# Kernel tuning notes

Measured on AMD Instinct MI355X. Metric: run time of the kernel, lower is better.

The kernel has to match this reference:

```python
import jax, jax.numpy as jnp
import numpy as np

N_NODES = 50000
N_EDGES = 800000
D_IN = 64
D_HID = 64
N_GRAPHS = 64


def setup_inputs() -> dict:
    key = jax.random.key(0)
    ks = jax.random.split(key, 10)
    x = jax.random.normal(ks[0], (N_NODES, D_IN), dtype=jnp.float32)
    edge_index = jax.random.randint(ks[1], (2, N_EDGES), 0, N_NODES, dtype=jnp.int64)
    batch = jnp.sort(jax.random.randint(ks[2], (N_NODES,), 0, N_GRAPHS, dtype=jnp.int64))
    s1 = 1.0 / np.sqrt(D_IN)
    s2 = 1.0 / np.sqrt(D_HID)
    W1 = jax.random.uniform(ks[3], (D_IN, D_HID), jnp.float32, -s1, s1)
    b1 = jnp.zeros((D_HID,), jnp.float32)
    W2 = jax.random.uniform(ks[4], (D_HID, D_HID), jnp.float32, -s2, s2)
    b2 = jnp.zeros((D_HID,), jnp.float32)
    W3 = jax.random.uniform(ks[5], (D_HID, D_HID), jnp.float32, -s2, s2)
    b3 = jnpp = jnp.zeros((D_HID,), jnp.float32)
    return {"x": x, "edge_index": edge_index, "batch": batch,
            "W1": W1, "b1": b1, "W2": W2, "b2": b2, "W3": W3, "b3": b3}


def _gcn_norm(edge_index, num_nodes):
    # add self-loops, then symmetric normalization deg^-1/2 A_hat deg^-1/2
    loop = jnp.arange(num_nodes, dtype=edge_index.dtype)
    row = jnp.concatenate([edge_index[0], loop])  # source
    col = jnp.concatenate([edge_index[1], loop])  # target (aggregation index)
    deg = jax.ops.segment_sum(jnp.ones_like(col, dtype=jnp.float32), col,
                              num_segments=num_nodes)
    dinv = jnp.where(deg > 0, jax.lax.rsqrt(deg), 0.0)
    norm = dinv[row] * dinv[col]  # [E+N]
    return row, col, norm


def _gcn_conv(x, row, col, norm, W, b, num_nodes):
    h = x @ W                                   # [N, D] small GEMM
    msg = h[row] * norm[:, None]                # edge-wise gather + scale
    out = jax.ops.segment_sum(msg, col, num_segments=num_nodes)  # scatter-add
    return out + b


def reference(x, edge_index, batch, W1, b1, W2, b2, W3, b3):
    n = x.shape[0]
    row, col, norm = _gcn_norm(edge_index, n)
    h = jax.nn.relu(_gcn_conv(x, row, col, norm, W1, b1, n))
    h = jax.nn.relu(_gcn_conv(h, row, col, norm, W2, b2, n))
    h = jax.nn.relu(_gcn_conv(h, row, col, norm, W3, b3, n))
    # global_mean_pool over graphs
    sums = jax.ops.segment_sum(h, batch, num_segments=N_GRAPHS)
    cnt = jax.ops.segment_sum(jnp.ones((n,), jnp.float32), batch,
                              num_segments=N_GRAPHS)
    return sums / jnp.maximum(cnt, 1.0)[:, None]
```

## Files before the change

kernel.cpp:

```cpp
#include <hip/hip_runtime.h>

#define N_NODES   50000
#define N_EDGES   800000
#define DF        64
#define N_GRAPHS  64
#define NPAD      50176

#define ABLK 200
#define AEDG (N_EDGES/ABLK)
#define RSH  9
#define NREG 98
#define RPAD 128
#define CAP  12288

__global__ __launch_bounds__(256)
void k_hist(const int* __restrict__ col, int* __restrict__ H,
            float* __restrict__ pool) {
    __shared__ int h[RPAD];
    const int t = threadIdx.x, b = blockIdx.x;
    if (b == 0)
        for (int i = t; i < N_GRAPHS * DF; i += 256) pool[i] = 0.f;
    if (t < RPAD) h[t] = 0;
    __syncthreads();
    const int e0 = b * AEDG;
    for (int i = t; i < AEDG; i += 256)
        atomicAdd(&h[col[e0 + i] >> RSH], 1);
    __syncthreads();
    if (t < RPAD) H[t * ABLK + b] = h[t];
}

__global__ __launch_bounds__(256)
void k_scanH(const int* __restrict__ H, int* __restrict__ O,
             int* __restrict__ T) {
    __shared__ int s[256];
    const int t = threadIdx.x, r = blockIdx.x;
    int v = (t < ABLK) ? H[r * ABLK + t] : 0;
    s[t] = v; __syncthreads();
    #pragma unroll
    for (int off = 1; off < 256; off <<= 1) {
        int x = (t >= off) ? s[t - off] : 0;
        __syncthreads();
        s[t] += x;
        __syncthreads();
    }
    if (t < ABLK) O[r * ABLK + t] = s[t] - v;
    if (t == 255) T[r] = s[255];
}

__global__ __launch_bounds__(256)
void k_bin(const int* __restrict__ row, const int* __restrict__ col,
           const int* __restrict__ O, const int* __restrict__ T,
           unsigned* __restrict__ staging) {
    __shared__ int cur[RPAD];
    __shared__ int rs[RPAD];
    const int t = threadIdx.x, b = blockIdx.x;
    int v = 0;
    if (t < RPAD) { v = T[t]; rs[t] = v; }
    __syncthreads();
    #pragma unroll
    for (int off = 1; off < RPAD; off <<= 1) {
        int x = 0;
        if (t < RPAD && t >= off) x = rs[t - off];
        __syncthreads();
        if (t < RPAD) rs[t] += x;
        __syncthreads();
    }
    if (t < RPAD) cur[t] = O[t * ABLK + b] + (rs[t] - v);
    __syncthreads();
    const int e0 = b * AEDG;
    for (int i = t; i < AEDG; i += 256) {
        int c = col[e0 + i];
        int rr = row[e0 + i];
        int slot = atomicAdd(&cur[c >> RSH], 1);
        staging[slot] = ((unsigned)c << 16) | (unsigned)rr;
    }
}

__global__ __launch_bounds__(512)
void k_csr(const unsigned* __restrict__ staging, const int* __restrict__ T,
           int* __restrict__ offs, float* __restrict__ dinv,
           int* __restrict__ esrc) {
    __shared__ int hist[512];
    __shared__ int cur[512];
    __shared__ int img[CAP];
    __shared__ int rs[RPAD];
    __shared__ int sh_s0, sh_s1;
    const int t = threadIdx.x, r = blockIdx.x;
    int v = 0;
    if (t < RPAD) { v = T[t]; rs[t] = v; }
    __syncthreads();
    #pragma unroll
    for (int off = 1; off < RPAD; off <<= 1) {
        int x = 0;
        if (t < RPAD && t >= off) x = rs[t - off];
        __syncthreads();
        if (t < RPAD) rs[t] += x;
        __syncthreads();
    }
    if (t == r) { sh_s0 = rs[t] - v; sh_s1 = rs[t]; }
    hist[t] = 0;
    __syncthreads();
    const int s0 = sh_s0, s1 = sh_s1;
    for (int i = s0 + t; i < s1; i += 512) {
        int ln = (int)(staging[i] >> 16) - (r << RSH);
        atomicAdd(&hist[ln], 1);
    }
    __syncthreads();
    int myc = hist[t];
    #pragma unroll
    for (int off = 1; off < 512; off <<= 1) {
        int x = (t >= off) ? hist[t - off] : 0;
        __syncthreads();
        hist[t] += x;
        __syncthreads();
    }
    int excl = hist[t] - myc;
    int n = (r << RSH) + t;
    offs[n] = s0 + excl;
    if (n < N_NODES) dinv[n] = rsqrtf((float)(myc + 1));
    cur[t] = excl;
    __syncthreads();
    for (int i = s0 + t; i < s1; i += 512) {
        unsigned p = staging[i];
        int ln = (int)(p >> 16) - (r << RSH);
        int rr = (int)(p & 0xFFFFu);
        int slot = atomicAdd(&cur[ln], 1);
        if (slot < CAP) img[slot] = rr;
        else           esrc[s0 + slot] = rr;
    }
    __syncthreads();
    int cnt = s1 - s0; if (cnt > CAP) cnt = CAP;
    for (int j = t; j < cnt; j += 512) esrc[s0 + j] = img[j];
}

#define GB_ROWS 64
#define LDX 68

__global__ __launch_bounds__(256)
void k_gemm(const float* __restrict__ in, const float* __restrict__ W,
            const float* __restrict__ bias, float* __restrict__ out,
            int relu_out) {
    __shared__ float XsT[DF][LDX];
    __shared__ float Ws[DF][DF];

    const int t = threadIdx.x;
    const int row0 = blockIdx.x * GB_ROWS;

    for (int idx = t * 4; idx < DF * DF; idx += 256 * 4) {
        float4 w = *(const float4*)&W[idx];
        Ws[idx >> 6][(idx & 63) + 0] = w.x;
        Ws[idx >> 6][(idx & 63) + 1] = w.y;
        Ws[idx >> 6][(idx & 63) + 2] = w.z;
        Ws[idx >> 6][(idx & 63) + 3] = w.w;
    }

    {
        const int r  = t >> 2;
        const int k0 = (t & 3) * 16;
        const int gr = row0 + r;
        const bool valid = gr < N_NODES;
        #pragma unroll
        for (int kk = 0; kk < 16; kk += 4) {
            float4 v = valid ? *(const float4*)&in[gr * DF + k0 + kk]
                             : make_float4(0.f, 0.f, 0.f, 0.f);
            XsT[k0 + kk + 0][r] = v.x;
            XsT[k0 + kk + 1][r] = v.y;
            XsT[k0 + kk + 2][r] = v.z;
            XsT[k0 + kk + 3][r] = v.w;
        }
    }
    __syncthreads();

    const int i = (t & 15) * 4;
    const int j = (t >> 4) * 4;
    float acc[4][4] = {};
    #pragma unroll 8
    for (int k = 0; k < DF; ++k) {
        float4 xv = *(const float4*)&XsT[k][i];
        float4 wv = *(const float4*)&Ws[k][j];
        acc[0][0] += xv.x * wv.x; acc[0][1] += xv.x * wv.y;
        acc[0][2] += xv.x * wv.z; acc[0][3] += xv.x * wv.w;
        acc[1][0] += xv.y * wv.x; acc[1][1] += xv.y * wv.y;
        acc[1][2] += xv.y * wv.z; acc[1][3] += xv.y * wv.w;
        acc[2][0] += xv.z * wv.x; acc[2][1] += xv.z * wv.y;
        acc[2][2] += xv.z * wv.z; acc[2][3] += xv.z * wv.w;
        acc[3][0] += xv.w * wv.x; acc[3][1] += xv.w * wv.y;
        acc[3][2] += xv.w * wv.z; acc[3][3] += xv.w * wv.w;
    }
    float4 bb = *(const float4*)&bias[j];
    #pragma unroll
    for (int u = 0; u < 4; ++u) {
        int gr = row0 + i + u;
        if (gr < N_NODES) {
            float4 o;
            o.x = acc[u][0] + bb.x;
            o.y = acc[u][1] + bb.y;
            o.z = acc[u][2] + bb.z;
            o.w = acc[u][3] + bb.w;
            if (relu_out) {
                o.x = o.x > 0.f ? o.x : 0.f;
                o.y = o.y > 0.f ? o.y : 0.f;
                o.z = o.z > 0.f ? o.z : 0.f;
                o.w = o.w > 0.f ? o.w : 0.f;
            }
            *(float4*)&out[gr * DF + j] = o;
        }
    }
}

__global__ __launch_bounds__(256)
void k_gather(const int* __restrict__ offs, const int* __restrict__ esrc,
              const float* __restrict__ dinv, const float* __restrict__ h,
              float* __restrict__ agg) {
    const int n = blockIdx.x * 4 + (threadIdx.x >> 6);
    if (n >= N_NODES) return;
    const int l = threadIdx.x & 63;
    const int g = l >> 4;
    const int q = l & 15;

    const float dc = dinv[n];
    float ax = 0.f, ay = 0.f, az = 0.f, aw = 0.f;

    if (g == 0) {
        float4 xv = *(const float4*)&h[n * DF + q * 4];
        ax = xv.x * dc; ay = xv.y * dc; az = xv.z * dc; aw = xv.w * dc;
    }

    const int s1 = offs[n + 1];
    int s = offs[n];
    for (; s + 16 <= s1; s += 16) {
        int r0 = esrc[s + g];
        int r1 = esrc[s + 4 + g];
        int r2 = esrc[s + 8 + g];
        int r3 = esrc[s + 12 + g];
        float w0 = dinv[r0], w1 = dinv[r1], w2 = dinv[r2], w3 = dinv[r3];
        float4 v0 = *(const float4*)&h[r0 * DF + q * 4];
        float4 v1 = *(const float4*)&h[r1 * DF + q * 4];
        float4 v2 = *(const float4*)&h[r2 * DF + q * 4];
        float4 v3 = *(const float4*)&h[r3 * DF + q * 4];
        ax += v0.x * w0; ay += v0.y * w0; az += v0.z * w0; aw += v0.w * w0;
        ax += v1.x * w1; ay += v1.y * w1; az += v1.z * w1; aw += v1.w * w1;
        ax += v2.x * w2; ay += v2.y * w2; az += v2.z * w2; aw += v2.w * w2;
        ax += v3.x * w3; ay += v3.y * w3; az += v3.z * w3; aw += v3.w * w3;
    }
    for (; s + 8 <= s1; s += 8) {
        int r0 = esrc[s + g];
        int r1 = esrc[s + 4 + g];
        float w0 = dinv[r0], w1 = dinv[r1];
        float4 v0 = *(const float4*)&h[r0 * DF + q * 4];
        float4 v1 = *(const float4*)&h[r1 * DF + q * 4];
        ax += v0.x * w0; ay += v0.y * w0; az += v0.z * w0; aw += v0.w * w0;
        ax += v1.x * w1; ay += v1.y * w1; az += v1.z * w1; aw += v1.w * w1;
    }
    for (; s < s1; s += 4) {
        int idx = s + g;
        bool valid = idx < s1;
        int r = valid ? esrc[idx] : n;
        float w = valid ? dinv[r] : 0.f;
        float4 v = *(const float4*)&h[r * DF + q * 4];
        ax += v.x * w; ay += v.y * w; az += v.z * w; aw += v.w * w;
    }

    ax += __shfl_xor(ax, 16); ay += __shfl_xor(ay, 16);
    az += __shfl_xor(az, 16); aw += __shfl_xor(aw, 16);
    ax += __shfl_xor(ax, 32); ay += __shfl_xor(ay, 32);
    az += __shfl_xor(az, 32); aw += __shfl_xor(aw, 32);

    if (l < 16)
        *(float4*)&agg[n * DF + q * 4] =
            make_float4(ax * dc, ay * dc, az * dc, aw * dc);
}

#define PNW 16

__global__ __launch_bounds__(256)
void k_pool2(const float* __restrict__ h, const int* __restrict__ batch,
             float* __restrict__ pool) {
    const int wave = threadIdx.x >> 6;
    const int d    = threadIdx.x & 63;
    int n0 = (blockIdx.x * 4 + wave) * PNW;
    if (n0 >= N_NODES) return;
    int n1 = n0 + PNW; if (n1 > N_NODES) n1 = N_NODES;
    float acc = 0.f;
    int g = batch[n0];
    for (int n = n0; n < n1; ++n) {
        int bg = batch[n];
        if (bg != g) {
            atomicAdd(&pool[g * DF + d], acc);
            acc = 0.f; g = bg;
        }
        acc += h[n * DF + d];
    }
    atomicAdd(&pool[g * DF + d], acc);
}

__device__ __forceinline__ int lb(const int* a, int n, int key) {
    int lo = 0, hi = n;
    while (lo < hi) { int m = (lo + hi) >> 1; if (a[m] < key) lo = m + 1; else hi = m; }
    return lo;
}

__global__ void k_div(const float* __restrict__ pool, const int* __restrict__ batch,
                      float* __restrict__ out) {
    int idx = blockIdx.x * blockDim.x + threadIdx.x;
    if (idx < N_GRAPHS * DF) {
        int g = idx >> 6;
        int c = lb(batch, N_NODES, g + 1) - lb(batch, N_NODES, g);
        out[idx] = pool[idx] / fmaxf((float)c, 1.0f);
    }
}


extern "C" void kernel_launch(void* const* d_in, const int* in_sizes, int n_in,
                              void* d_out, int out_size, void* d_ws, size_t ws_size,
                              hipStream_t stream) {
    const float* x     = (const float*)d_in[0];
    const int*   ei    = (const int*)d_in[1];
    const int*   batch = (const int*)d_in[2];
    const float* W1    = (const float*)d_in[3];
    const float* b1    = (const float*)d_in[4];
    const float* W2    = (const float*)d_in[5];
    const float* b2    = (const float*)d_in[6];
    const float* W3    = (const float*)d_in[7];
    const float* b3    = (const float*)d_in[8];
    float* out = (float*)d_out;

    const int* row = ei;
    const int* col = ei + N_EDGES;

    char* wsb = (char*)d_ws;
    float*    pool    = (float*)wsb;
    int*      H       = (int*)(pool + N_GRAPHS * DF);
    int*      O       = H + RPAD * ABLK;
    int*      T       = O + RPAD * ABLK;
    int*      offs    = T + RPAD;
    int*      esrc    = offs + NPAD;
    unsigned* staging = (unsigned*)(esrc + N_EDGES);
    float*    dinv    = (float*)(staging + N_EDGES);
    float*    bufA    = dinv + NPAD;
    float*    bufB    = bufA + N_NODES * DF;

    const int nblk_G  = (N_NODES + GB_ROWS - 1) / GB_ROWS;
    const int nblk_GA = (N_NODES + 3) / 4;
    const int nblk_P  = (N_NODES + 4 * PNW - 1) / (4 * PNW);

    k_hist<<<ABLK, 256, 0, stream>>>(col, H, pool);
    k_scanH<<<RPAD, 256, 0, stream>>>(H, O, T);
    k_bin<<<ABLK, 256, 0, stream>>>(row, col, O, T, staging);
    k_csr<<<NREG, 512, 0, stream>>>(staging, T, offs, dinv, esrc);

    k_gather<<<nblk_GA, 256, 0, stream>>>(offs, esrc, dinv, x, bufA);
    k_gemm<<<nblk_G, 256, 0, stream>>>(bufA, W1, b1, bufB, 1);
    k_gather<<<nblk_GA, 256, 0, stream>>>(offs, esrc, dinv, bufB, bufA);
    k_gemm<<<nblk_G, 256, 0, stream>>>(bufA, W2, b2, bufB, 1);
    k_gather<<<nblk_GA, 256, 0, stream>>>(offs, esrc, dinv, bufB, bufA);
    k_gemm<<<nblk_G, 256, 0, stream>>>(bufA, W3, b3, bufB, 1);

    k_pool2<<<nblk_P, 256, 0, stream>>>(bufB, batch, pool);
    k_div<<<(N_GRAPHS * DF + 255) / 256, 256, 0, stream>>>(pool, batch, out);
}
```

Baseline: 262.8 us.

## Fuse gather aggregation with GEMM per layer and fold mean-pool into last layer

Each GCN layer's neighbour gather now writes its aggregated rows straight into shared memory, and the 64x64 GEMM runs on them in the same 512-thread block. This removes the intermediate aggregation buffer round trip and halves the kernel launches. The last layer also accumulates the ReLU outputs into per-graph pool sums through shared-memory atomics, which removes the separate pool kernel and the store of the final activations. In exchange each block processes its 64 nodes serially (8 per wave), which may reduce latency hiding in the gather.

```diff
diff --git a/kernel.cpp b/kernel.cpp
--- a/kernel.cpp
+++ b/kernel.cpp
@@ -133,165 +133,167 @@
     for (int j = t; j < cnt; j += 512) esrc[s0 + j] = img[j];
 }
 
-#define GB_ROWS 64
+#define FB_ROWS 64
+#define NPW 8
 #define LDX 68
 
-__global__ __launch_bounds__(256)
-void k_gemm(const float* __restrict__ in, const float* __restrict__ W,
-            const float* __restrict__ bias, float* __restrict__ out,
-            int relu_out) {
+__global__ __launch_bounds__(512, 4)
+void k_fused(const int* __restrict__ offs, const int* __restrict__ esrc,
+             const float* __restrict__ dinv, const float* __restrict__ h,
+             const float* __restrict__ W, const float* __restrict__ bias,
+             float* __restrict__ out, const int* __restrict__ batch,
+             float* __restrict__ pool) {
     __shared__ float XsT[DF][LDX];
     __shared__ float Ws[DF][DF];
+    __shared__ float plocal[4 * DF];
+    __shared__ int   sh_batch[FB_ROWS];
 
     const int t = threadIdx.x;
-    const int row0 = blockIdx.x * GB_ROWS;
-
-    for (int idx = t * 4; idx < DF * DF; idx += 256 * 4) {
+    const int row0 = blockIdx.x * FB_ROWS;
+
+    for (int idx = t * 4; idx < DF * DF; idx += 512 * 4) {
         float4 w = *(const float4*)&W[idx];
         Ws[idx >> 6][(idx & 63) + 0] = w.x;
         Ws[idx >> 6][(idx & 63) + 1] = w.y;
         Ws[idx >> 6][(idx & 63) + 2] = w.z;
         Ws[idx >> 6][(idx & 63) + 3] = w.w;
     }
-
-    {
-        const int r  = t >> 2;
-        const int k0 = (t & 3) * 16;
-        const int gr = row0 + r;
-        const bool valid = gr < N_NODES;
-        #pragma unroll
-        for (int kk = 0; kk < 16; kk += 4) {
-            float4 v = valid ? *(const float4*)&in[gr * DF + k0 + kk]
-                             : make_float4(0.f, 0.f, 0.f, 0.f);
-            XsT[k0 + kk + 0][r] = v.x;
-            XsT[k0 + kk + 1][r] = v.y;
-            XsT[k0 + kk + 2][r] = v.z;
-            XsT[k0 + kk + 3][r] = v.w;
+    if (pool) {
+        if (t < 4 * DF) plocal[t] = 0.f;
+        if (t < FB_ROWS) {
+            int n = row0 + t;
+            sh_batch[t] = batch[n < N_NODES ? n : N_NODES - 1];
+        }
+    }
+
+    const int wv = t >> 6;
+    const int l  = t & 63;
+    const int g  = l >> 4;
+    const int q  = l & 15;
+    for (int ii = 0; ii < NPW; ++ii) {
+        const int r = wv * NPW + ii;
+        const int n = row0 + r;
+        if (n >= N_NODES) break;
+
+        const float dc = dinv[n];
+        float ax = 0.f, ay = 0.f, az = 0.f, aw = 0.f;
+
+        if (g == 0) {
+            float4 xv = *(const float4*)&h[n * DF + q * 4];
+            ax = xv.x * dc; ay = xv.y * dc; az = xv.z * dc; aw = xv.w * dc;
+        }
+
+        const int s1 = offs[n + 1];
+        int s = offs[n];
+        for (; s + 16 <= s1; s += 16) {
+            int r0 = esrc[s + g];
+            int r1 = esrc[s + 4 + g];
+            int r2 = esrc[s + 8 + g];
+            int r3 = esrc[s + 12 + g];
+            float w0 = dinv[r0], w1 = dinv[r1], w2 = dinv[r2], w3 = dinv[r3];
+            float4 v0 = *(const float4*)&h[r0 * DF + q * 4];
+            float4 v1 = *(const float4*)&h[r1 * DF + q * 4];
+            float4 v2 = *(const float4*)&h[r2 * DF + q * 4];
+            float4 v3 = *(const float4*)&h[r3 * DF + q * 4];
+            ax += v0.x * w0; ay += v0.y * w0; az += v0.z * w0; aw += v0.w * w0;
+            ax += v1.x * w1; ay += v1.y * w1; az += v1.z * w1; aw += v1.w * w1;
+            ax += v2.x * w2; ay += v2.y * w2; az += v2.z * w2; aw += v2.w * w2;
+            ax += v3.x * w3; ay += v3.y * w3; az += v3.z * w3; aw += v3.w * w3;
+        }
+        for (; s + 8 <= s1; s += 8) {
+            int r0 = esrc[s + g];
+            int r1 = esrc[s + 4 + g];
+            float w0 = dinv[r0], w1 = dinv[r1];
+            float4 v0 = *(const float4*)&h[r0 * DF + q * 4];
+            float4 v1 = *(const float4*)&h[r1 * DF + q * 4];
+            ax += v0.x * w0; ay += v0.y * w0; az += v0.z * w0; aw += v0.w * w0;
+            ax += v1.x * w1; ay += v1.y * w1; az += v1.z * w1; aw += v1.w * w1;
+        }
+        for (; s < s1; s += 4) {
+            int idx = s + g;
+            bool valid = idx < s1;
+            int rr = valid ? esrc[idx] : n;
+            float w = valid ? dinv[rr] : 0.f;
+            float4 v = *(const float4*)&h[rr * DF + q * 4];
+            ax += v.x * w; ay += v.y * w; az += v.z * w; aw += v.w * w;
+        }
+
+        ax += __shfl_xor(ax, 16); ay += __shfl_xor(ay, 16);
+        az += __shfl_xor(az, 16); aw += __shfl_xor(aw, 16);
+        ax += __shfl_xor(ax, 32); ay += __shfl_xor(ay, 32);
+        az += __shfl_xor(az, 32); aw += __shfl_xor(aw, 32);
+
+        if (l < 16) {
+            XsT[q * 4 + 0][r] = ax * dc;
+            XsT[q * 4 + 1][r] = ay * dc;
+            XsT[q * 4 + 2][r] = az * dc;
+            XsT[q * 4 + 3][r] = aw * dc;
         }
     }
     __syncthreads();
 
     const int i = (t & 15) * 4;
-    const int j = (t >> 4) * 4;
-    float acc[4][4] = {};
+    const int j = (t >> 4) * 2;
+    float acc[4][2] = {};
     #pragma unroll 8
     for (int k = 0; k < DF; ++k) {
         float4 xv = *(const float4*)&XsT[k][i];
-        float4 wv = *(const float4*)&Ws[k][j];
-        acc[0][0] += xv.x * wv.x; acc[0][1] += xv.x * wv.y;
-        acc[0][2] += xv.x * wv.z; acc[0][3] += xv.x * wv.w;
-        acc[1][0] += xv.y * wv.x; acc[1][1] += xv.y * wv.y;
-        acc[1][2] += xv.y * wv.z; acc[1][3] += xv.y * wv.w;
-        acc[2][0] += xv.z * wv.x; acc[2][1] += xv.z * wv.y;
-        acc[2][2] += xv.z * wv.z; acc[2][3] += xv.z * wv.w;
-        acc[3][0] += xv.w * wv.x; acc[3][1] += xv.w * wv.y;
-        acc[3][2] += xv.w * wv.z; acc[3][3] += xv.w * wv.w;
-    }
-    float4 bb = *(const float4*)&bias[j];
-    #pragma unroll
-    for (int u = 0; u < 4; ++u) {
-        int gr = row0 + i + u;
-        if (gr < N_NODES) {
-            float4 o;
-            o.x = acc[u][0] + bb.x;
-            o.y = acc[u][1] + bb.y;
-            o.z = acc[u][2] + bb.z;
-            o.w = acc[u][3] + bb.w;
-            if (relu_out) {
-                o.x = o.x > 0.f ? o.x : 0.f;
-                o.y = o.y > 0.f ? o.y : 0.f;
-                o.z = o.z > 0.f ? o.z : 0.f;
-                o.w = o.w > 0.f ? o.w : 0.f;
+        float2 wvv = *(const float2*)&Ws[k][j];
+        acc[0][0] += xv.x * wvv.x; acc[0][1] += xv.x * wvv.y;
+        acc[1][0] += xv.y * wvv.x; acc[1][1] += xv.y * wvv.y;
+        acc[2][0] += xv.z * wvv.x; acc[2][1] += xv.z * wvv.y;
+        acc[3][0] += xv.w * wvv.x; acc[3][1] += xv.w * wvv.y;
+    }
+    const float bx = bias[j], by = bias[j + 1];
+
+    if (!pool) {
+        #pragma unroll
+        for (int u = 0; u < 4; ++u) {
+            int gr = row0 + i + u;
+            if (gr < N_NODES) {
+                float ox = acc[u][0] + bx;
+                float oy = acc[u][1] + by;
+                ox = ox > 0.f ? ox : 0.f;
+                oy = oy > 0.f ? oy : 0.f;
+                *(float2*)&out[gr * DF + j] = make_float2(ox, oy);
             }
-            *(float4*)&out[gr * DF + j] = o;
-        }
-    }
-}
-
-__global__ __launch_bounds__(256)
-void k_gather(const int* __restrict__ offs, const int* __restrict__ esrc,
-              const float* __restrict__ dinv, const float* __restrict__ h,
-              float* __restrict__ agg) {
-    const int n = blockIdx.x * 4 + (threadIdx.x >> 6);
-    if (n >= N_NODES) return;
-    const int l = threadIdx.x & 63;
-    const int g = l >> 4;
-    const int q = l & 15;
-
-    const float dc = dinv[n];
-    float ax = 0.f, ay = 0.f, az = 0.f, aw = 0.f;
-
-    if (g == 0) {
-        float4 xv = *(const float4*)&h[n * DF + q * 4];
-        ax = xv.x * dc; ay = xv.y * dc; az = xv.z * dc; aw = xv.w * dc;
-    }
-
-    const int s1 = offs[n + 1];
-    int s = offs[n];
-    for (; s + 16 <= s1; s += 16) {
-        int r0 = esrc[s + g];
-        int r1 = esrc[s + 4 + g];
-        int r2 = esrc[s + 8 + g];
-        int r3 = esrc[s + 12 + g];
-        float w0 = dinv[r0], w1 = dinv[r1], w2 = dinv[r2], w3 = dinv[r3];
-        float4 v0 = *(const float4*)&h[r0 * DF + q * 4];
-        float4 v1 = *(const float4*)&h[r1 * DF + q * 4];
-        float4 v2 = *(const float4*)&h[r2 * DF + q * 4];
-        float4 v3 = *(const float4*)&h[r3 * DF + q * 4];
-        ax += v0.x * w0; ay += v0.y * w0; az += v0.z * w0; aw += v0.w * w0;
-        ax += v1.x * w1; ay += v1.y * w1; az += v1.z * w1; aw += v1.w * w1;
-        ax += v2.x * w2; ay += v2.y * w2; az += v2.z * w2; aw += v2.w * w2;
-        ax += v3.x * w3; ay += v3.y * w3; az += v3.z * w3; aw += v3.w * w3;
-    }
-    for (; s + 8 <= s1; s += 8) {
-        int r0 = esrc[s + g];
-        int r1 = esrc[s + 4 + g];
-        float w0 = dinv[r0], w1 = dinv[r1];
-        float4 v0 = *(const float4*)&h[r0 * DF + q * 4];
-        float4 v1 = *(const float4*)&h[r1 * DF + q * 4];
-        ax += v0.x * w0; ay += v0.y * w0; az += v0.z * w0; aw += v0.w * w0;
-        ax += v1.x * w1; ay += v1.y * w1; az += v1.z * w1; aw += v1.w * w1;
-    }
-    for (; s < s1; s += 4) {
-        int idx = s + g;
-        bool valid = idx < s1;
-        int r = valid ? esrc[idx] : n;
-        float w = valid ? dinv[r] : 0.f;
-        float4 v = *(const float4*)&h[r * DF + q * 4];
-        ax += v.x * w; ay += v.y * w; az += v.z * w; aw += v.w * w;
-    }
-
-    ax += __shfl_xor(ax, 16); ay += __shfl_xor(ay, 16);
-    az += __shfl_xor(az, 16); aw += __shfl_xor(aw, 16);
-    ax += __shfl_xor(ax, 32); ay += __shfl_xor(ay, 32);
-    az += __shfl_xor(az, 32); aw += __shfl_xor(aw, 32);
-
-    if (l < 16)
-        *(float4*)&agg[n * DF + q * 4] =
-            make_float4(ax * dc, ay * dc, az * dc, aw * dc);
-}
-
-#define PNW 16
-
-__global__ __launch_bounds__(256)
-void k_pool2(const float* __restrict__ h, const int* __restrict__ batch,
-             float* __restrict__ pool) {
-    const int wave = threadIdx.x >> 6;
-    const int d    = threadIdx.x & 63;
-    int n0 = (blockIdx.x * 4 + wave) * PNW;
-    if (n0 >= N_NODES) return;
-    int n1 = n0 + PNW; if (n1 > N_NODES) n1 = N_NODES;
-    float acc = 0.f;
-    int g = batch[n0];
-    for (int n = n0; n < n1; ++n) {
-        int bg = batch[n];
-        if (bg != g) {
-            atomicAdd(&pool[g * DF + d], acc);
-            acc = 0.f; g = bg;
-        }
-        acc += h[n * DF + d];
-    }
-    atomicAdd(&pool[g * DF + d], acc);
+        }
+    } else {
+        const int g0 = sh_batch[0];
+        const int span = sh_batch[FB_ROWS - 1] - g0 + 1;
+        if (span <= 4) {
+            #pragma unroll
+            for (int u = 0; u < 4; ++u) {
+                int gr = row0 + i + u;
+                if (gr < N_NODES) {
+                    float ox = acc[u][0] + bx;
+                    float oy = acc[u][1] + by;
+                    ox = ox > 0.f ? ox : 0.f;
+                    oy = oy > 0.f ? oy : 0.f;
+                    int gl = sh_batch[i + u] - g0;
+                    atomicAdd(&plocal[gl * DF + j],     ox);
+                    atomicAdd(&plocal[gl * DF + j + 1], oy);
+                }
+            }
+            __syncthreads();
+            for (int idx = t; idx < span * DF; idx += 512)
+                atomicAdd(&pool[g0 * DF + idx], plocal[idx]);
+        } else {
+            #pragma unroll
+            for (int u = 0; u < 4; ++u) {
+                int gr = row0 + i + u;
+                if (gr < N_NODES) {
+                    float ox = acc[u][0] + bx;
+                    float oy = acc[u][1] + by;
+                    ox = ox > 0.f ? ox : 0.f;
+                    oy = oy > 0.f ? oy : 0.f;
+                    int gg = sh_batch[i + u];
+                    atomicAdd(&pool[gg * DF + j],     ox);
+                    atomicAdd(&pool[gg * DF + j + 1], oy);
+                }
+            }
+        }
+    }
 }
 
 __device__ __forceinline__ int lb(const int* a, int n, int key) {
@@ -340,22 +342,19 @@
     float*    bufA    = dinv + NPAD;
     float*    bufB    = bufA + N_NODES * DF;
 
-    const int nblk_G  = (N_NODES + GB_ROWS - 1) / GB_ROWS;
-    const int nblk_GA = (N_NODES + 3) / 4;
-    const int nblk_P  = (N_NODES + 4 * PNW - 1) / (4 * PNW);
+    const int nblk_F = (N_NODES + FB_ROWS - 1) / FB_ROWS;
 
     k_hist<<<ABLK, 256, 0, stream>>>(col, H, pool);
     k_scanH<<<RPAD, 256, 0, stream>>>(H, O, T);
     k_bin<<<ABLK, 256, 0, stream>>>(row, col, O, T, staging);
     k_csr<<<NREG, 512, 0, stream>>>(staging, T, offs, dinv, esrc);
 
-    k_gather<<<nblk_GA, 256, 0, stream>>>(offs, esrc, dinv, x, bufA);
-    k_gemm<<<nblk_G, 256, 0, stream>>>(bufA, W1, b1, bufB, 1);
-    k_gather<<<nblk_GA, 256, 0, stream>>>(offs, esrc, dinv, bufB, bufA);
-    k_gemm<<<nblk_G, 256, 0, stream>>>(bufA, W2, b2, bufB, 1);
-    k_gather<<<nblk_GA, 256, 0, stream>>>(offs, esrc, dinv, bufB, bufA);
-    k_gemm<<<nblk_G, 256, 0, stream>>>(bufA, W3, b3, bufB, 1);
-
-    k_pool2<<<nblk_P, 256, 0, stream>>>(bufB, batch, pool);
+    k_fused<<<nblk_F, 512, 0, stream>>>(offs, esrc, dinv, x,    W1, b1, bufA,
+                                        nullptr, nullptr);
+    k_fused<<<nblk_F, 512, 0, stream>>>(offs, esrc, dinv, bufA, W2, b2, bufB,
+                                        nullptr, nullptr);
+    k_fused<<<nblk_F, 512, 0, stream>>>(offs, esrc, dinv, bufB, W3, b3, nullptr,
+                                        batch, pool);
+
     k_div<<<(N_GRAPHS * DF + 255) / 256, 256, 0, stream>>>(pool, batch, out);
 }
```

After: 262.5 us. No clear change (-0.1%).
